# Performance work log

Hardware: AMD Instinct MI355X
Metric: run time of the kernel (lower is better)

## Reference

```python
import jax, jax.numpy as jnp
import numpy as np

P = 64        # patch size
DIM = 128     # embed dim
ROT = 64      # rotary dim (dim_head)
REC = 3       # recurrence
T = 15        # max_seq_len == conv channels
PPP = 1 * P * P  # pixels per patch


def rope_tables(H):
    # rotary-embedding-torch: inv_freq over even indices, angles repeated pairwise
    inv = 1.0 / (10000.0 ** (jnp.arange(0, ROT, 2, dtype=jnp.float32) / ROT))
    ang = jnp.arange(H, dtype=jnp.float32)[:, None] * inv[None, :]   # [H, ROT//2]
    ang = jnp.repeat(ang, 2, axis=-1)                                 # [H, ROT]
    return jnp.cos(ang), jnp.sin(ang)


def apply_rope(t, cos, sin):
    # t: [B, C, H, W]; rotate first ROT features along seq dim H
    tl = t[..., :ROT]
    x2 = tl.reshape(tl.shape[:-1] + (ROT // 2, 2))
    rot = jnp.stack([-x2[..., 1], x2[..., 0]], axis=-1).reshape(tl.shape)
    tl = tl * cos + rot * sin  # cos/sin [H, ROT] broadcast over [B, C, H, ROT]
    return jnp.concatenate([tl, t[..., ROT:]], axis=-1)


def criss_cross(x, Wq, bq, Wk, bk, Wv, bv, gamma, cos, sin, diag_mask):
    # x: [B, C, H, W] with C=T, H=n_patches, W=DIM
    q = jnp.einsum('bchw,oc->bohw', x, Wq) + bq[None, :, None, None]
    k = jnp.einsum('bchw,oc->bohw', x, Wk) + bk[None, :, None, None]
    v = jnp.einsum('bchw,oc->bohw', x, Wv) + bv[None, :, None, None]
    q = apply_rope(q, cos, sin)[:, 0]  # [B, H, W] (q/k have a single channel)
    k = apply_rope(k, cos, sin)[:, 0]
    H = x.shape[2]
    # energy_H[b,h,w,g] = q[b,h,w] * k[b,g,w]  (column attention, diag masked -inf)
    eH = jnp.einsum('bhw,bgw->bhwg', q, k) + diag_mask[None, :, None, :]
    # energy_W[b,h,w,u] = q[b,h,w] * k[b,h,u]  (row attention)
    eW = jnp.einsum('bhw,bhu->bhwu', q, k)
    att = jax.nn.softmax(jnp.concatenate([eH, eW], axis=-1), axis=-1)
    attH, attW = att[..., :H], att[..., H:]
    outH = jnp.einsum('bcgw,bhwg->bchw', v, attH)
    outW = jnp.einsum('bchu,bhwu->bchw', v, attW)
    return gamma * (outH + outW) + x


def setup_inputs() -> dict:
    key = jax.random.key(0)
    ks = jax.random.split(key, 16)
    f = lambda k, shape, s=0.05: jax.random.normal(k, shape, jnp.float32) * s
    x = jax.random.normal(ks[0], (2, T, 1, 1024, 1024), jnp.float32)
    return dict(
        x=x,
        W_emb=f(ks[1], (PPP, DIM)), b_emb=f(ks[2], (DIM,)),
        Wq=f(ks[3], (REC, 1, T)), bq=f(ks[4], (REC, 1)),
        Wk=f(ks[5], (REC, 1, T)), bk=f(ks[6], (REC, 1)),
        Wv=f(ks[7], (REC, T, T)), bv=f(ks[8], (REC, T)),
        gamma=jax.random.normal(ks[9], (REC,), jnp.float32) * 0.5,
        W_mlp=f(ks[10], (DIM, DIM)),
        W_p1=f(ks[11], (DIM, DIM)), b_p1=f(ks[12], (DIM,)),
        W_p2=f(ks[13], (DIM, PPP)), b_p2=f(ks[14], (PPP,)),
    )


def reference(x, W_emb, b_emb, Wq, bq, Wk, bk, Wv, bv, gamma, W_mlp, W_p1, b_p1, W_p2, b_p2):
    b, t, c, Hi, Wi = x.shape
    nh, nw = Hi // P, Wi // P
    Hn = nh * nw  # number of patches
    # patchify: b t c (h p1)(w p2) -> b t (h w) (c p1 p2)
    patches = x.reshape(b, t, c, nh, P, nw, P).transpose(0, 1, 3, 5, 2, 4, 6)
    patches = patches.reshape(b, t, Hn, c * P * P)
    x_e = patches @ W_emb + b_emb  # [b, t, Hn, DIM]

    cos, sin = rope_tables(Hn)
    diag_mask = jnp.where(jnp.eye(Hn, dtype=bool), -jnp.inf, 0.0).astype(jnp.float32)
    h = x_e  # interpreted as [B=b, C=t, H=Hn, W=DIM]
    for i in range(REC):
        h = criss_cross(h, Wq[i], bq[i], Wk[i], bk[i], Wv[i], bv[i], gamma[i], cos, sin, diag_mask)
    x_h = h @ W_mlp  # Linear(dim, dim, bias=False)

    def recover(z):
        p = (z @ W_p1 + b_p1) @ W_p2 + b_p2          # [b, t, Hn, PPP]
        return p.reshape(b, t, c, Hi, Wi)             # b t (d h w) -> b t d h w

    x_p = recover(x_e)
    x_h_p = recover(x_h)
    return (x_e, x_h, x_p, x_h_p)
```

## Files before the change

kernel.cpp:

```cpp
#include <hip/hip_runtime.h>
#include <math.h>

typedef __attribute__((ext_vector_type(8))) short bf16x8;
typedef __attribute__((ext_vector_type(8))) unsigned short u16x8;
typedef __attribute__((ext_vector_type(4))) unsigned short u16x4;
typedef __attribute__((ext_vector_type(4))) float f32x4;
typedef unsigned short u16;

#define XE_OFF   0
#define XH_OFF   983040
#define XP_OFF   1966080
#define XHP_OFF  33423360

#define SCR_COS   0
#define SCR_SIN   8192
#define SCR_Q     16384
#define SCR_K     81920
#define SCR_V     147456
#define SCR_HA    1130496
#define SCR_HB    2113536
#define SCR_M1    3096576
#define SCR_S1    3162112
#define SCR_AW    3227648
#define SCR_VT    4210688
#define SCR_KT    5193728
#define SCR_QT    5259264
#define SCR_OHT   5324800
#define SCR_M2    6307840
#define SCR_S2    6373376
#define SCR_PART  6438912

__device__ __forceinline__ u16 f2bf(float f) {
    unsigned u = __float_as_uint(f);
    return (u16)((u + 0x7fffu + ((u >> 16) & 1)) >> 16);
}

union U8 { u16 h[8]; bf16x8 v; u16x8 u; };

__global__ __launch_bounds__(256) void prep_k(const float* __restrict__ Wemb,
                                              const float* __restrict__ Wp1,
                                              const float* __restrict__ Wmlp,
                                              const float* __restrict__ Wp2,
                                              float* __restrict__ cosb, float* __restrict__ sinb,
                                              u16* __restrict__ Wembt, u16* __restrict__ Wp1t,
                                              u16* __restrict__ Wmlpt, u16* __restrict__ Wp2t) {
    __shared__ float tl[32][33];
    int bid = blockIdx.x, tid = threadIdx.x;
    if (bid < 32) {
        int i = bid * 256 + tid;
        int n = i >> 5, j = i & 31;
        float inv = expf(-(float)j * 0.28782313662425573f);
        float ang = (float)n * inv;
        cosb[i] = cosf(ang);
        sinb[i] = sinf(ang);
        return;
    }
    const float* in; u16* outp; int K, N, gx, gy;
    if (bid < 544)      { int i = bid - 32;  in = Wemb; outp = Wembt; K = 4096; N = 128;  gx = i & 3;   gy = i >> 2; }
    else if (bid < 560) { int i = bid - 544; in = Wp1;  outp = Wp1t;  K = 128;  N = 128;  gx = i & 3;   gy = i >> 2; }
    else if (bid < 576) { int i = bid - 560; in = Wmlp; outp = Wmlpt; K = 128;  N = 128;  gx = i & 3;   gy = i >> 2; }
    else                { int i = bid - 576; in = Wp2;  outp = Wp2t;  K = 128;  N = 4096; gx = i & 127; gy = i >> 7; }
    int n0 = gx * 32, k0 = gy * 32;
    int tx = tid & 31, ty = tid >> 5;
#pragma unroll
    for (int r = 0; r < 4; ++r)
        tl[ty + r * 8][tx] = in[(size_t)(k0 + ty + r * 8) * N + n0 + tx];
    __syncthreads();
#pragma unroll
    for (int r = 0; r < 4; ++r)
        outp[(size_t)(n0 + ty + r * 8) * K + k0 + tx] = f2bf(tl[tx][ty + r * 8]);
}

__global__ __launch_bounds__(256) void embed_mfma_k(const float* __restrict__ x,
                                                    const u16* __restrict__ Wembt,
                                                    float* __restrict__ part) {
    __shared__ char Al[64 * 128];
    __shared__ char Bl[128 * 128];
    int ck = blockIdx.x, mt = blockIdx.y;
    int m0 = mt * 64;
    int bt = m0 >> 8;
    int n0r = m0 & 255;
    const float* xb = x + (size_t)bt * 1048576;
    int tid = threadIdx.x;
    int ln = tid & 63, wv = tid >> 6;
    int wm = wv >> 1, wn = wv & 1;

    f32x4 acc[2][4];
#pragma unroll
    for (int mi = 0; mi < 2; ++mi)
#pragma unroll
        for (int ni = 0; ni < 4; ++ni) acc[mi][ni] = (f32x4){0.f, 0.f, 0.f, 0.f};

    int ar = tid & 63, aseg = tid >> 6;
    int an = n0r + ar;
    const float* arow = xb + ((size_t)(an >> 4) * 64) * 1024 + (an & 15) * 64;

    for (int bk = 0; bk < 8; ++bk) {
        int kbase = ck * 512 + bk * 64;
        __syncthreads();
        {
            const float* src = arow + (size_t)(kbase >> 6) * 1024 + aseg * 16;
            float4 f0 = ((const float4*)src)[0];
            float4 f1 = ((const float4*)src)[1];
            float4 f2 = ((const float4*)src)[2];
            float4 f3 = ((const float4*)src)[3];
            U8 u0, u1;
            u0.h[0] = f2bf(f0.x); u0.h[1] = f2bf(f0.y); u0.h[2] = f2bf(f0.z); u0.h[3] = f2bf(f0.w);
            u0.h[4] = f2bf(f1.x); u0.h[5] = f2bf(f1.y); u0.h[6] = f2bf(f1.z); u0.h[7] = f2bf(f1.w);
            u1.h[0] = f2bf(f2.x); u1.h[1] = f2bf(f2.y); u1.h[2] = f2bf(f2.z); u1.h[3] = f2bf(f2.w);
            u1.h[4] = f2bf(f3.x); u1.h[5] = f2bf(f3.y); u1.h[6] = f2bf(f3.z); u1.h[7] = f2bf(f3.w);
            int sw = (ar & 7) << 4;
            *(bf16x8*)(Al + ar * 128 + ((aseg * 32) ^ sw))      = u0.v;
            *(bf16x8*)(Al + ar * 128 + ((aseg * 32 + 16) ^ sw)) = u1.v;
        }
#pragma unroll
        for (int j = 0; j < 4; ++j) {
            int c = tid + 256 * j;
            int n = c >> 3, k0 = (c & 7) * 8;
            U8 u;
            u.u = *(const u16x8*)(Wembt + (size_t)n * 4096 + kbase + k0);
            *(bf16x8*)(Bl + n * 128 + ((k0 * 2) ^ ((n & 7) << 4))) = u.v;
        }
        __syncthreads();
#pragma unroll
        for (int ks = 0; ks < 2; ++ks) {
            int k2 = (ks * 32 + (ln >> 4) * 8) * 2;
            bf16x8 a[2], b[4];
#pragma unroll
            for (int mi = 0; mi < 2; ++mi) {
                int row = wm * 32 + mi * 16 + (ln & 15);
                a[mi] = *(const bf16x8*)(Al + row * 128 + (k2 ^ ((row & 7) << 4)));
            }
#pragma unroll
            for (int ni = 0; ni < 4; ++ni) {
                int n = wn * 64 + ni * 16 + (ln & 15);
                b[ni] = *(const bf16x8*)(Bl + n * 128 + (k2 ^ ((n & 7) << 4)));
            }
#pragma unroll
            for (int mi = 0; mi < 2; ++mi)
#pragma unroll
                for (int ni = 0; ni < 4; ++ni)
                    acc[mi][ni] = __builtin_amdgcn_mfma_f32_16x16x32_bf16(a[mi], b[ni], acc[mi][ni], 0, 0, 0);
        }
    }
    float* p = part + (size_t)ck * 983040;
#pragma unroll
    for (int mi = 0; mi < 2; ++mi)
#pragma unroll
        for (int ni = 0; ni < 4; ++ni)
#pragma unroll
            for (int r = 0; r < 4; ++r) {
                int row = m0 + wm * 32 + mi * 16 + (ln >> 4) * 4 + r;
                int col = wn * 64 + ni * 16 + (ln & 15);
                p[(size_t)row * 128 + col] = acc[mi][ni][r];
            }
}

__global__ __launch_bounds__(256) void embed_reduce_k(const float* __restrict__ part,
                                                      const float* __restrict__ bemb,
                                                      float* __restrict__ xe) {
    int i = blockIdx.x * 256 + threadIdx.x;
    const float4* p = (const float4*)part;
    float4 s = p[i];
#pragma unroll
    for (int j = 1; j < 8; ++j) {
        float4 a = p[(size_t)j * 245760 + i];
        s.x += a.x; s.y += a.y; s.z += a.z; s.w += a.w;
    }
    float4 bb = ((const float4*)bemb)[i & 31];
    s.x += bb.x; s.y += bb.y; s.z += bb.z; s.w += bb.w;
    ((float4*)xe)[i] = s;
}

template<int ABF, int OBF, int HASB>
__global__ __launch_bounds__(256) void gemm_bt_k(const void* __restrict__ Ap,
                                                 const u16* __restrict__ Bt,
                                                 const float* __restrict__ bias,
                                                 void* __restrict__ outp, int N) {
    __shared__ char Al[64 * 256];
    __shared__ char Bl[128 * 256];
    int n0 = blockIdx.x * 128, m0 = blockIdx.y * 64;
    int tid = threadIdx.x;
    int ln = tid & 63, wv = tid >> 6;
    int wm = wv >> 1, wn = wv & 1;
    {
        int row = tid >> 2, kseg = (tid & 3) * 32;
        int sw = (row & 7) << 4;
        if (ABF) {
            const u16* src = (const u16*)Ap + (size_t)(m0 + row) * 128 + kseg;
#pragma unroll
            for (int j = 0; j < 4; ++j) {
                U8 u; u.u = *(const u16x8*)(src + j * 8);
                *(bf16x8*)(Al + row * 256 + (((kseg + j * 8) * 2) ^ sw)) = u.v;
            }
        } else {
            const float* src = (const float*)Ap + (size_t)(m0 + row) * 128 + kseg;
#pragma unroll
            for (int j = 0; j < 4; ++j) {
                float4 f0 = ((const float4*)src)[2 * j];
                float4 f1 = ((const float4*)src)[2 * j + 1];
                U8 u;
                u.h[0] = f2bf(f0.x); u.h[1] = f2bf(f0.y); u.h[2] = f2bf(f0.z); u.h[3] = f2bf(f0.w);
                u.h[4] = f2bf(f1.x); u.h[5] = f2bf(f1.y); u.h[6] = f2bf(f1.z); u.h[7] = f2bf(f1.w);
                *(bf16x8*)(Al + row * 256 + (((kseg + j * 8) * 2) ^ sw)) = u.v;
            }
        }
    }
    {
        int n = tid >> 1, kseg = (tid & 1) * 64;
        int sw = (n & 7) << 4;
        const u16* src = Bt + (size_t)(n0 + n) * 128 + kseg;
#pragma unroll
        for (int j = 0; j < 8; ++j) {
            U8 u; u.u = *(const u16x8*)(src + j * 8);
            *(bf16x8*)(Bl + n * 256 + (((kseg + j * 8) * 2) ^ sw)) = u.v;
        }
    }
    __syncthreads();
    f32x4 acc[2][4];
#pragma unroll
    for (int mi = 0; mi < 2; ++mi)
#pragma unroll
        for (int ni = 0; ni < 4; ++ni) acc[mi][ni] = (f32x4){0.f, 0.f, 0.f, 0.f};
#pragma unroll
    for (int ks = 0; ks < 4; ++ks) {
        int k2 = (ks * 32 + (ln >> 4) * 8) * 2;
        bf16x8 a[2], b[4];
#pragma unroll
        for (int mi = 0; mi < 2; ++mi) {
            int row = wm * 32 + mi * 16 + (ln & 15);
            a[mi] = *(const bf16x8*)(Al + row * 256 + (k2 ^ ((row & 7) << 4)));
        }
#pragma unroll
        for (int ni = 0; ni < 4; ++ni) {
            int n = wn * 64 + ni * 16 + (ln & 15);
            b[ni] = *(const bf16x8*)(Bl + n * 256 + (k2 ^ ((n & 7) << 4)));
        }
#pragma unroll
        for (int mi = 0; mi < 2; ++mi)
#pragma unroll
            for (int ni = 0; ni < 4; ++ni)
                acc[mi][ni] = __builtin_amdgcn_mfma_f32_16x16x32_bf16(a[mi], b[ni], acc[mi][ni], 0, 0, 0);
    }
#pragma unroll
    for (int mi = 0; mi < 2; ++mi)
#pragma unroll
        for (int ni = 0; ni < 4; ++ni)
#pragma unroll
            for (int r = 0; r < 4; ++r) {
                int row = m0 + wm * 32 + mi * 16 + (ln >> 4) * 4 + r;
                int col = n0 + wn * 64 + ni * 16 + (ln & 15);
                float v = acc[mi][ni][r];
                if (HASB) v += bias[col];
                if (OBF) ((u16*)outp)[(size_t)row * N + col] = f2bf(v);
                else     ((float*)outp)[(size_t)row * N + col] = v;
            }
}

__global__ __launch_bounds__(256) void recover_k(const float* __restrict__ A,
                                                 const u16* __restrict__ Wp1t,
                                                 const float* __restrict__ bp1,
                                                 const u16* __restrict__ Wp2t,
                                                 const float* __restrict__ bp2,
                                                 float* __restrict__ outp) {
    __shared__ char Zl[64 * 256];
    __shared__ char Bl[128 * 256];
    __shared__ char Al2[64 * 256];
    int cb = blockIdx.x * 512, m0 = blockIdx.y * 64;
    int tid = threadIdx.x, ln = tid & 63, wv = tid >> 6;
    int wm = wv >> 1, wn = wv & 1;
    {
        int row = tid >> 2, kseg = (tid & 3) * 32;
        int sw = (row & 7) << 4;
        const float* src = A + (size_t)(m0 + row) * 128 + kseg;
#pragma unroll
        for (int j = 0; j < 4; ++j) {
            float4 f0 = ((const float4*)src)[2 * j];
            float4 f1 = ((const float4*)src)[2 * j + 1];
            U8 u;
            u.h[0] = f2bf(f0.x); u.h[1] = f2bf(f0.y); u.h[2] = f2bf(f0.z); u.h[3] = f2bf(f0.w);
            u.h[4] = f2bf(f1.x); u.h[5] = f2bf(f1.y); u.h[6] = f2bf(f1.z); u.h[7] = f2bf(f1.w);
            *(bf16x8*)(Al2 + row * 256 + (((kseg + j * 8) * 2) ^ sw)) = u.v;
        }
        int n = tid >> 1, ks2 = (tid & 1) * 64;
        int swb = (n & 7) << 4;
        const u16* bsrc = Wp1t + (size_t)n * 128 + ks2;
#pragma unroll
        for (int j = 0; j < 8; ++j) {
            U8 u; u.u = *(const u16x8*)(bsrc + j * 8);
            *(bf16x8*)(Bl + n * 256 + (((ks2 + j * 8) * 2) ^ swb)) = u.v;
        }
    }
    __syncthreads();
    {
        f32x4 zacc[2][4];
#pragma unroll
        for (int mi = 0; mi < 2; ++mi)
#pragma unroll
            for (int ni = 0; ni < 4; ++ni) zacc[mi][ni] = (f32x4){0.f, 0.f, 0.f, 0.f};
#pragma unroll
        for (int ks = 0; ks < 4; ++ks) {
            int k2 = (ks * 32 + (ln >> 4) * 8) * 2;
            bf16x8 a[2], b[4];
#pragma unroll
            for (int mi = 0; mi < 2; ++mi) {
                int row = wm * 32 + mi * 16 + (ln & 15);
                a[mi] = *(const bf16x8*)(Al2 + row * 256 + (k2 ^ ((row & 7) << 4)));
            }
#pragma unroll
            for (int ni = 0; ni < 4; ++ni) {
                int n = wn * 64 + ni * 16 + (ln & 15);
                b[ni] = *(const bf16x8*)(Bl + n * 256 + (k2 ^ ((n & 7) << 4)));
            }
#pragma unroll
            for (int mi = 0; mi < 2; ++mi)
#pragma unroll
                for (int ni = 0; ni < 4; ++ni)
                    zacc[mi][ni] = __builtin_amdgcn_mfma_f32_16x16x32_bf16(a[mi], b[ni], zacc[mi][ni], 0, 0, 0);
        }
#pragma unroll
        for (int ni = 0; ni < 4; ++ni) {
            int col = wn * 64 + ni * 16 + (ln & 15);
            float bb = bp1[col];
#pragma unroll
            for (int mi = 0; mi < 2; ++mi)
#pragma unroll
                for (int r = 0; r < 4; ++r) {
                    int row = wm * 32 + mi * 16 + (ln >> 4) * 4 + r;
                    *(u16*)(Zl + row * 256 + ((col * 2) ^ ((row & 7) << 4))) =
                        f2bf(zacc[mi][ni][r] + bb);
                }
        }
    }
    for (int nb = 0; nb < 4; ++nb) {
        __syncthreads();
        {
            int n = tid >> 1, ks2 = (tid & 1) * 64;
            int swb = (n & 7) << 4;
            const u16* bsrc = Wp2t + (size_t)(cb + nb * 128 + n) * 128 + ks2;
#pragma unroll
            for (int j = 0; j < 8; ++j) {
                U8 u; u.u = *(const u16x8*)(bsrc + j * 8);
                *(bf16x8*)(Bl + n * 256 + (((ks2 + j * 8) * 2) ^ swb)) = u.v;
            }
        }
        __syncthreads();
        f32x4 acc[2][4];
#pragma unroll
        for (int mi = 0; mi < 2; ++mi)
#pragma unroll
            for (int ni = 0; ni < 4; ++ni) acc[mi][ni] = (f32x4){0.f, 0.f, 0.f, 0.f};
#pragma unroll
        for (int ks = 0; ks < 4; ++ks) {
            int k2 = (ks * 32 + (ln >> 4) * 8) * 2;
            bf16x8 a[2], b[4];
#pragma unroll
            for (int mi = 0; mi < 2; ++mi) {
                int row = wm * 32 + mi * 16 + (ln & 15);
                a[mi] = *(const bf16x8*)(Zl + row * 256 + (k2 ^ ((row & 7) << 4)));
            }
#pragma unroll
            for (int ni = 0; ni < 4; ++ni) {
                int n = wn * 64 + ni * 16 + (ln & 15);
                b[ni] = *(const bf16x8*)(Bl + n * 256 + (k2 ^ ((n & 7) << 4)));
            }
#pragma unroll
            for (int mi = 0; mi < 2; ++mi)
#pragma unroll
                for (int ni = 0; ni < 4; ++ni)
                    acc[mi][ni] = __builtin_amdgcn_mfma_f32_16x16x32_bf16(a[mi], b[ni], acc[mi][ni], 0, 0, 0);
        }
#pragma unroll
        for (int ni = 0; ni < 4; ++ni) {
            int col = cb + nb * 128 + wn * 64 + ni * 16 + (ln & 15);
            float bb = bp2[col];
#pragma unroll
            for (int mi = 0; mi < 2; ++mi)
#pragma unroll
                for (int r = 0; r < 4; ++r) {
                    int row = m0 + wm * 32 + mi * 16 + (ln >> 4) * 4 + r;
                    __builtin_nontemporal_store(acc[mi][ni][r] + bb,
                                                outp + (size_t)row * 4096 + col);
                }
        }
    }
}

__global__ __launch_bounds__(128) void qkvW_k(const float* __restrict__ hin,
    const float* __restrict__ Wq, const float* __restrict__ bq,
    const float* __restrict__ Wk, const float* __restrict__ bk,
    const float* __restrict__ Wv, const float* __restrict__ bv,
    const float* __restrict__ cosb, const float* __restrict__ sinb,
    float* __restrict__ q, float* __restrict__ k, float* __restrict__ v,
    float* __restrict__ m1g, float* __restrict__ S1g, float* __restrict__ accW) {
    __shared__ char Pl[128 * 256];
    __shared__ char Vt[16 * 256];
    __shared__ float klds[128];
    __shared__ float red[2];
    __shared__ float ol[128][17];
    int b = blockIdx.x >> 8, hh = blockIdx.x & 255;
    int d = threadIdx.x;
    float hv[15];
#pragma unroll
    for (int t = 0; t < 15; ++t)
        hv[t] = hin[(((size_t)b * 15 + t) * 256 + hh) * 128 + d];
    float qp = bq[0], kp = bk[0];
#pragma unroll
    for (int t = 0; t < 15; ++t) {
        qp = fmaf(hv[t], Wq[t], qp);
        kp = fmaf(hv[t], Wk[t], kp);
    }
    float qpart = __shfl_xor(qp, 1);
    float kpart = __shfl_xor(kp, 1);
    float qo = qp, ko = kp;
    if (d < 64) {
        int j = d >> 1;
        float c = cosb[hh * 32 + j], s = sinb[hh * 32 + j];
        if (d & 1) { qo = fmaf(qp, c,  qpart * s); ko = fmaf(kp, c,  kpart * s); }
        else       { qo = fmaf(qp, c, -qpart * s); ko = fmaf(kp, c, -kpart * s); }
    }
    float vv[15];
#pragma unroll
    for (int c = 0; c < 15; ++c) {
        float a = bv[c];
#pragma unroll
        for (int t = 0; t < 15; ++t) a = fmaf(hv[t], Wv[c * 15 + t], a);
        vv[c] = a;
    }
    q[((size_t)b * 256 + hh) * 128 + d] = qo;
    k[((size_t)b * 256 + hh) * 128 + d] = ko;
#pragma unroll
    for (int c = 0; c < 15; ++c)
        v[(((size_t)b * 15 + c) * 256 + hh) * 128 + d] = vv[c];
    klds[d] = ko;
#pragma unroll
    for (int c = 0; c < 15; ++c)
        *(u16*)(Vt + ((c * 256 + d * 2) ^ ((c & 7) << 4))) = f2bf(vv[c]);
    *(u16*)(Vt + ((15 * 256 + d * 2) ^ 112)) = 0x3F80;
    float ka = fabsf(ko);
#pragma unroll
    for (int off = 32; off >= 1; off >>= 1) ka = fmaxf(ka, __shfl_xor(ka, off));
    if ((d & 63) == 0) red[d >> 6] = ka;
    __syncthreads();
    ka = fmaxf(red[0], red[1]);
    float m1 = fabsf(qo) * ka;
    m1g[((size_t)b * 256 + hh) * 128 + d] = m1;
    int swp = (d & 7) << 4;
#pragma unroll 4
    for (int u8 = 0; u8 < 128; u8 += 8) {
        f32x4 k0 = *(const f32x4*)&klds[u8];
        f32x4 k1 = *(const f32x4*)&klds[u8 + 4];
        U8 u;
        u.h[0] = f2bf(__expf(fmaf(qo, k0.x, -m1)));
        u.h[1] = f2bf(__expf(fmaf(qo, k0.y, -m1)));
        u.h[2] = f2bf(__expf(fmaf(qo, k0.z, -m1)));
        u.h[3] = f2bf(__expf(fmaf(qo, k0.w, -m1)));
        u.h[4] = f2bf(__expf(fmaf(qo, k1.x, -m1)));
        u.h[5] = f2bf(__expf(fmaf(qo, k1.y, -m1)));
        u.h[6] = f2bf(__expf(fmaf(qo, k1.z, -m1)));
        u.h[7] = f2bf(__expf(fmaf(qo, k1.w, -m1)));
        *(bf16x8*)(Pl + d * 256 + ((u8 * 2) ^ swp)) = u.v;
    }
    __syncthreads();
    int ln = d & 63, wvv = d >> 6;
    f32x4 acc[4];
#pragma unroll
    for (int mt = 0; mt < 4; ++mt) acc[mt] = (f32x4){0.f, 0.f, 0.f, 0.f};
#pragma unroll
    for (int ks = 0; ks < 4; ++ks) {
        int k2 = (ks * 32 + (ln >> 4) * 8) * 2;
        int n = ln & 15;
        bf16x8 bf = *(const bf16x8*)(Vt + n * 256 + (k2 ^ ((n & 7) << 4)));
#pragma unroll
        for (int mt = 0; mt < 4; ++mt) {
            int row = wvv * 64 + mt * 16 + (ln & 15);
            bf16x8 a = *(const bf16x8*)(Pl + row * 256 + (k2 ^ ((row & 7) << 4)));
            acc[mt] = __builtin_amdgcn_mfma_f32_16x16x32_bf16(a, bf, acc[mt], 0, 0, 0);
        }
    }
    {
        int c = ln & 15;
#pragma unroll
        for (int mt = 0; mt < 4; ++mt)
#pragma unroll
            for (int r = 0; r < 4; ++r)
                ol[wvv * 64 + mt * 16 + (ln >> 4) * 4 + r][c] = acc[mt][r];
    }
    __syncthreads();
    S1g[((size_t)b * 256 + hh) * 128 + d] = ol[d][15];
#pragma unroll
    for (int c = 0; c < 15; ++c)
        accW[(((size_t)b * 15 + c) * 256 + hh) * 128 + d] = ol[d][c];
}

__global__ __launch_bounds__(256) void trans_k(const float* __restrict__ v,
                                               const float* __restrict__ k,
                                               const float* __restrict__ q,
                                               float* __restrict__ vT,
                                               float* __restrict__ kT,
                                               float* __restrict__ qT) {
    __shared__ float tl[32][33];
    int bid = blockIdx.x, tid = threadIdx.x;
    const float* in; float* outp; int tile;
    if (bid < 960)       { int idx = bid >> 5; tile = bid & 31; in = v + (size_t)idx * 32768; outp = vT + (size_t)idx * 32768; }
    else if (bid < 1024) { int i = bid - 960;  int idx = i >> 5; tile = i & 31; in = k + (size_t)idx * 32768; outp = kT + (size_t)idx * 32768; }
    else                 { int i = bid - 1024; int idx = i >> 5; tile = i & 31; in = q + (size_t)idx * 32768; outp = qT + (size_t)idx * 32768; }
    int g0 = (tile >> 2) * 32, w0 = (tile & 3) * 32;
    int tx = tid & 31, ty = tid >> 5;
#pragma unroll
    for (int r = 0; r < 4; ++r)
        tl[ty + 8 * r][tx] = in[(size_t)(g0 + ty + 8 * r) * 128 + w0 + tx];
    __syncthreads();
#pragma unroll
    for (int r = 0; r < 4; ++r)
        outp[(size_t)(w0 + ty + 8 * r) * 256 + g0 + tx] = tl[tx][ty + 8 * r];
}

__global__ __launch_bounds__(256) void attnH_k(const float* __restrict__ qT,
    const float* __restrict__ kT, const float* __restrict__ vT,
    float* __restrict__ outHT, float* __restrict__ m2T, float* __restrict__ S2T) {
    __shared__ char Pl[256 * 128];
    __shared__ char Vl[16 * 128];
    __shared__ float klds[256];
    __shared__ float ol[256][17];
    __shared__ float kabs_s;
    int b = blockIdx.x >> 7, w = blockIdx.x & 127;
    int tid = threadIdx.x;
    if (tid < 64) {
        f32x4 kk = *(const f32x4*)(kT + ((size_t)b * 128 + w) * 256 + 4 * tid);
        *(f32x4*)&klds[4 * tid] = kk;
        float ka = fmaxf(fmaxf(fabsf(kk.x), fabsf(kk.y)), fmaxf(fabsf(kk.z), fabsf(kk.w)));
#pragma unroll
        for (int off = 32; off >= 1; off >>= 1) ka = fmaxf(ka, __shfl_xor(ka, off));
        if (tid == 0) kabs_s = ka;
    }
    float qs = qT[((size_t)b * 128 + w) * 256 + tid];
    __syncthreads();
    float m2 = fabsf(qs) * kabs_s;
    int ln = tid & 63, wv = tid >> 6;
    f32x4 acc[4];
#pragma unroll
    for (int mt = 0; mt < 4; ++mt) acc[mt] = (f32x4){0.f, 0.f, 0.f, 0.f};
    int swp = (tid & 7) << 4;
    for (int gc = 0; gc < 4; ++gc) {
        {
            int c = tid >> 4, seg = tid & 15;
            int gg = gc * 64 + seg * 4;
            u16x4 o;
            if (c < 15) {
                f32x4 vv4 = *(const f32x4*)(vT + (((size_t)b * 15 + c) * 128 + w) * 256 + gg);
                o[0] = f2bf(vv4.x); o[1] = f2bf(vv4.y); o[2] = f2bf(vv4.z); o[3] = f2bf(vv4.w);
            } else {
                o[0] = 0x3F80; o[1] = 0x3F80; o[2] = 0x3F80; o[3] = 0x3F80;
            }
            *(u16x4*)(Vl + ((c * 128 + seg * 8) ^ ((c & 7) << 4))) = o;
        }
#pragma unroll
        for (int g8 = 0; g8 < 64; g8 += 8) {
            f32x4 k0 = *(const f32x4*)&klds[gc * 64 + g8];
            f32x4 k1 = *(const f32x4*)&klds[gc * 64 + g8 + 4];
            int gbase = gc * 64 + g8;
            U8 u;
            float p0 = __expf(fmaf(qs, k0.x, -m2)); if (gbase + 0 == tid) p0 = 0.f;
            float p1 = __expf(fmaf(qs, k0.y, -m2)); if (gbase + 1 == tid) p1 = 0.f;
            float p2 = __expf(fmaf(qs, k0.z, -m2)); if (gbase + 2 == tid) p2 = 0.f;
            float p3 = __expf(fmaf(qs, k0.w, -m2)); if (gbase + 3 == tid) p3 = 0.f;
            float p4 = __expf(fmaf(qs, k1.x, -m2)); if (gbase + 4 == tid) p4 = 0.f;
            float p5 = __expf(fmaf(qs, k1.y, -m2)); if (gbase + 5 == tid) p5 = 0.f;
            float p6 = __expf(fmaf(qs, k1.z, -m2)); if (gbase + 6 == tid) p6 = 0.f;
            float p7 = __expf(fmaf(qs, k1.w, -m2)); if (gbase + 7 == tid) p7 = 0.f;
            u.h[0] = f2bf(p0); u.h[1] = f2bf(p1); u.h[2] = f2bf(p2); u.h[3] = f2bf(p3);
            u.h[4] = f2bf(p4); u.h[5] = f2bf(p5); u.h[6] = f2bf(p6); u.h[7] = f2bf(p7);
            *(bf16x8*)(Pl + tid * 128 + ((g8 * 2) ^ swp)) = u.v;
        }
        __syncthreads();
#pragma unroll
        for (int ks = 0; ks < 2; ++ks) {
            int k2 = (ks * 32 + (ln >> 4) * 8) * 2;
            int n = ln & 15;
            bf16x8 bf = *(const bf16x8*)(Vl + n * 128 + (k2 ^ ((n & 7) << 4)));
#pragma unroll
            for (int mt = 0; mt < 4; ++mt) {
                int row = wv * 64 + mt * 16 + (ln & 15);
                bf16x8 a = *(const bf16x8*)(Pl + row * 128 + (k2 ^ ((row & 7) << 4)));
                acc[mt] = __builtin_amdgcn_mfma_f32_16x16x32_bf16(a, bf, acc[mt], 0, 0, 0);
            }
        }
        __syncthreads();
    }
    {
        int c = ln & 15;
#pragma unroll
        for (int mt = 0; mt < 4; ++mt)
#pragma unroll
            for (int r = 0; r < 4; ++r)
                ol[wv * 64 + mt * 16 + (ln >> 4) * 4 + r][c] = acc[mt][r];
    }
    __syncthreads();
    size_t base = ((size_t)b * 128 + w) * 256 + tid;
    m2T[base] = m2;
    S2T[base] = ol[tid][15];
#pragma unroll
    for (int c = 0; c < 15; ++c)
        outHT[(((size_t)b * 15 + c) * 128 + w) * 256 + tid] = ol[tid][c];
}

__global__ __launch_bounds__(256) void combine_k(const float* __restrict__ hin,
    const float* __restrict__ accW, const float* __restrict__ outHT,
    const float* __restrict__ m1, const float* __restrict__ S1,
    const float* __restrict__ m2T, const float* __restrict__ S2T,
    const float* __restrict__ gptr, float* __restrict__ hout) {
    __shared__ float ot[32][33];
    __shared__ float m2l[32][33], s2l[32][33];
    int bid = blockIdx.x;
    int c = bid % 15, wt = (bid / 15) & 3, ht = (bid / 60) & 7, b = bid / 480;
    int h0 = ht * 32, w0 = wt * 32;
    int tid = threadIdx.x, tx = tid & 31, ty = tid >> 5;
#pragma unroll
    for (int r = 0; r < 4; ++r) {
        int wl = ty + 8 * r;
        size_t tb = ((size_t)b * 128 + w0 + wl) * 256 + h0 + tx;
        m2l[wl][tx] = m2T[tb];
        s2l[wl][tx] = S2T[tb];
        ot[wl][tx] = outHT[(((size_t)b * 15 + c) * 128 + w0 + wl) * 256 + h0 + tx];
    }
    __syncthreads();
    float g = gptr[0];
#pragma unroll
    for (int r = 0; r < 4; ++r) {
        int hl = ty + 8 * r;
        int h = h0 + hl, w = w0 + tx;
        size_t hw = ((size_t)b * 256 + h) * 128 + w;
        float m1v = m1[hw], S1v = S1[hw];
        float m2v = m2l[tx][hl], S2v = s2l[tx][hl];
        float mm = fmaxf(m1v, m2v);
        float e1 = __expf(m1v - mm), e2 = __expf(m2v - mm);
        float sc = g / (S1v * e1 + S2v * e2);
        size_t oi = (((size_t)b * 15 + c) * 256 + h) * 128 + w;
        hout[oi] = hin[oi] + sc * e1 * accW[oi] + sc * e2 * ot[tx][hl];
    }
}

extern "C" void kernel_launch(void* const* d_in, const int* in_sizes, int n_in,
                              void* d_out, int out_size, void* d_ws, size_t ws_size,
                              hipStream_t stream) {
    const float* x    = (const float*)d_in[0];
    const float* Wemb = (const float*)d_in[1];
    const float* bemb = (const float*)d_in[2];
    const float* Wq   = (const float*)d_in[3];
    const float* bq   = (const float*)d_in[4];
    const float* Wk   = (const float*)d_in[5];
    const float* bk   = (const float*)d_in[6];
    const float* Wv   = (const float*)d_in[7];
    const float* bv   = (const float*)d_in[8];
    const float* gam  = (const float*)d_in[9];
    const float* Wmlp = (const float*)d_in[10];
    const float* Wp1  = (const float*)d_in[11];
    const float* bp1  = (const float*)d_in[12];
    const float* Wp2  = (const float*)d_in[13];
    const float* bp2  = (const float*)d_in[14];

    float* out = (float*)d_out;
    float* xe  = out + XE_OFF;
    float* xh  = out + XH_OFF;
    float* xp  = out + XP_OFF;
    float* xhp = out + XHP_OFF;

    float* scr   = xhp;
    float* cosb  = scr + SCR_COS;
    float* sinb  = scr + SCR_SIN;
    float* qb    = scr + SCR_Q;
    float* kb    = scr + SCR_K;
    float* vb    = scr + SCR_V;
    float* ha    = scr + SCR_HA;
    float* hb    = scr + SCR_HB;
    float* m1g   = scr + SCR_M1;
    float* S1g   = scr + SCR_S1;
    float* accW  = scr + SCR_AW;
    float* vTb   = scr + SCR_VT;
    float* kTb   = scr + SCR_KT;
    float* qTb   = scr + SCR_QT;
    float* outHT = scr + SCR_OHT;
    float* m2T   = scr + SCR_M2;
    float* S2T   = scr + SCR_S2;
    float* prt   = scr + SCR_PART;
    u16* Wp2t  = (u16*)d_ws;
    u16* Wembt = (u16*)((char*)d_ws + 1048576);
    u16* Wp1t  = (u16*)((char*)d_ws + 2097152);
    u16* Wmlpt = (u16*)((char*)d_ws + 2129920);

    prep_k<<<1088, 256, 0, stream>>>(Wemb, Wp1, Wmlp, Wp2, cosb, sinb,
                                     Wembt, Wp1t, Wmlpt, Wp2t);
    embed_mfma_k<<<dim3(8, 120), 256, 0, stream>>>(x, Wembt, prt);
    embed_reduce_k<<<960, 256, 0, stream>>>(prt, bemb, xe);

    const float* hin = xe;
    float* houts[3] = {ha, hb, ha};
    for (int i = 0; i < 3; ++i) {
        qkvW_k<<<512, 128, 0, stream>>>(hin, Wq + i * 15, bq + i, Wk + i * 15, bk + i,
                                        Wv + i * 225, bv + i * 15, cosb, sinb,
                                        qb, kb, vb, m1g, S1g, accW);
        trans_k<<<1088, 256, 0, stream>>>(vb, kb, qb, vTb, kTb, qTb);
        attnH_k<<<256, 256, 0, stream>>>(qTb, kTb, vTb, outHT, m2T, S2T);
        combine_k<<<1536, 256, 0, stream>>>(hin, accW, outHT, m1g, S1g, m2T, S2T,
                                            gam + i, houts[i]);
        hin = houts[i];
    }

    gemm_bt_k<0, 0, 0><<<dim3(1, 120), 256, 0, stream>>>(hin, Wmlpt, nullptr, xh, 128);
    recover_k<<<dim3(8, 120), 256, 0, stream>>>(xe, Wp1t, bp1, Wp2t, bp2, xp);
    recover_k<<<dim3(8, 120), 256, 0, stream>>>(xh, Wp1t, bp1, Wp2t, bp2, xhp);
}
```

Before: 232.3 us.

## Split attention kernels across more threads and blocks for occupancy

qkvW_k now runs 256 threads per block: one half computes q/k with RoPE while the other computes v, and the exp/MFMA work is split between the halves. attnH_k splits the key dimension into two halves across twice as many blocks. Each half writes its own partial output and sum buffers, and combine_k adds them. This raises parallelism on a GPU that is underfilled with only 256–512 blocks, at the cost of extra scratch traffic and an additional read in combine.

```diff
diff --git a/kernel.cpp b/kernel.cpp
--- a/kernel.cpp
+++ b/kernel.cpp
@@ -28,7 +28,9 @@
 #define SCR_OHT   5324800
 #define SCR_M2    6307840
 #define SCR_S2    6373376
-#define SCR_PART  6438912
+#define SCR_OHT1  6438912
+#define SCR_S21   7421952
+#define SCR_PART  7487488
 
 __device__ __forceinline__ u16 f2bf(float f) {
     unsigned u = __float_as_uint(f);
@@ -386,7 +388,7 @@
     }
 }
 
-__global__ __launch_bounds__(128) void qkvW_k(const float* __restrict__ hin,
+__global__ __launch_bounds__(256) void qkvW_k(const float* __restrict__ hin,
     const float* __restrict__ Wq, const float* __restrict__ bq,
     const float* __restrict__ Wk, const float* __restrict__ bk,
     const float* __restrict__ Wv, const float* __restrict__ bv,
@@ -396,60 +398,73 @@
     __shared__ char Pl[128 * 256];
     __shared__ char Vt[16 * 256];
     __shared__ float klds[128];
+    __shared__ float qlds[128];
     __shared__ float red[2];
     __shared__ float ol[128][17];
     int b = blockIdx.x >> 8, hh = blockIdx.x & 255;
-    int d = threadIdx.x;
-    float hv[15];
-#pragma unroll
-    for (int t = 0; t < 15; ++t)
-        hv[t] = hin[(((size_t)b * 15 + t) * 256 + hh) * 128 + d];
-    float qp = bq[0], kp = bk[0];
-#pragma unroll
-    for (int t = 0; t < 15; ++t) {
-        qp = fmaf(hv[t], Wq[t], qp);
-        kp = fmaf(hv[t], Wk[t], kp);
-    }
-    float qpart = __shfl_xor(qp, 1);
-    float kpart = __shfl_xor(kp, 1);
-    float qo = qp, ko = kp;
-    if (d < 64) {
-        int j = d >> 1;
-        float c = cosb[hh * 32 + j], s = sinb[hh * 32 + j];
-        if (d & 1) { qo = fmaf(qp, c,  qpart * s); ko = fmaf(kp, c,  kpart * s); }
-        else       { qo = fmaf(qp, c, -qpart * s); ko = fmaf(kp, c, -kpart * s); }
-    }
-    float vv[15];
-#pragma unroll
-    for (int c = 0; c < 15; ++c) {
-        float a = bv[c];
-#pragma unroll
-        for (int t = 0; t < 15; ++t) a = fmaf(hv[t], Wv[c * 15 + t], a);
-        vv[c] = a;
-    }
-    q[((size_t)b * 256 + hh) * 128 + d] = qo;
-    k[((size_t)b * 256 + hh) * 128 + d] = ko;
-#pragma unroll
-    for (int c = 0; c < 15; ++c)
-        v[(((size_t)b * 15 + c) * 256 + hh) * 128 + d] = vv[c];
-    klds[d] = ko;
-#pragma unroll
-    for (int c = 0; c < 15; ++c)
-        *(u16*)(Vt + ((c * 256 + d * 2) ^ ((c & 7) << 4))) = f2bf(vv[c]);
-    *(u16*)(Vt + ((15 * 256 + d * 2) ^ 112)) = 0x3F80;
-    float ka = fabsf(ko);
-#pragma unroll
-    for (int off = 32; off >= 1; off >>= 1) ka = fmaxf(ka, __shfl_xor(ka, off));
-    if ((d & 63) == 0) red[d >> 6] = ka;
-    __syncthreads();
-    ka = fmaxf(red[0], red[1]);
+    int tid = threadIdx.x;
+    int d = tid & 127, half = tid >> 7;
+
+    if (half == 0) {
+        float hv[15];
+#pragma unroll
+        for (int t = 0; t < 15; ++t)
+            hv[t] = hin[(((size_t)b * 15 + t) * 256 + hh) * 128 + d];
+        float qp = bq[0], kp = bk[0];
+#pragma unroll
+        for (int t = 0; t < 15; ++t) {
+            qp = fmaf(hv[t], Wq[t], qp);
+            kp = fmaf(hv[t], Wk[t], kp);
+        }
+        float qpart = __shfl_xor(qp, 1);
+        float kpart = __shfl_xor(kp, 1);
+        float qo = qp, ko = kp;
+        if (d < 64) {
+            int j = d >> 1;
+            float c = cosb[hh * 32 + j], s = sinb[hh * 32 + j];
+            if (d & 1) { qo = fmaf(qp, c,  qpart * s); ko = fmaf(kp, c,  kpart * s); }
+            else       { qo = fmaf(qp, c, -qpart * s); ko = fmaf(kp, c, -kpart * s); }
+        }
+        q[((size_t)b * 256 + hh) * 128 + d] = qo;
+        k[((size_t)b * 256 + hh) * 128 + d] = ko;
+        klds[d] = ko;
+        qlds[d] = qo;
+        float ka = fabsf(ko);
+#pragma unroll
+        for (int off = 32; off >= 1; off >>= 1) ka = fmaxf(ka, __shfl_xor(ka, off));
+        if ((tid & 63) == 0) red[tid >> 6] = ka;
+    } else {
+        float hv[15];
+#pragma unroll
+        for (int t = 0; t < 15; ++t)
+            hv[t] = hin[(((size_t)b * 15 + t) * 256 + hh) * 128 + d];
+        float vv[15];
+#pragma unroll
+        for (int c = 0; c < 15; ++c) {
+            float a = bv[c];
+#pragma unroll
+            for (int t = 0; t < 15; ++t) a = fmaf(hv[t], Wv[c * 15 + t], a);
+            vv[c] = a;
+        }
+#pragma unroll
+        for (int c = 0; c < 15; ++c)
+            v[(((size_t)b * 15 + c) * 256 + hh) * 128 + d] = vv[c];
+#pragma unroll
+        for (int c = 0; c < 15; ++c)
+            *(u16*)(Vt + ((c * 256 + d * 2) ^ ((c & 7) << 4))) = f2bf(vv[c]);
+        *(u16*)(Vt + ((15 * 256 + d * 2) ^ 112)) = 0x3F80;
+    }
+    __syncthreads();
+    float ka = fmaxf(red[0], red[1]);
+    float qo = qlds[d];
     float m1 = fabsf(qo) * ka;
-    m1g[((size_t)b * 256 + hh) * 128 + d] = m1;
+    if (half == 0) m1g[((size_t)b * 256 + hh) * 128 + d] = m1;
     int swp = (d & 7) << 4;
+    int u0 = half * 64;
 #pragma unroll 4
-    for (int u8 = 0; u8 < 128; u8 += 8) {
-        f32x4 k0 = *(const f32x4*)&klds[u8];
-        f32x4 k1 = *(const f32x4*)&klds[u8 + 4];
+    for (int u8 = 0; u8 < 64; u8 += 8) {
+        f32x4 k0 = *(const f32x4*)&klds[u0 + u8];
+        f32x4 k1 = *(const f32x4*)&klds[u0 + u8 + 4];
         U8 u;
         u.h[0] = f2bf(__expf(fmaf(qo, k0.x, -m1)));
         u.h[1] = f2bf(__expf(fmaf(qo, k0.y, -m1)));
@@ -459,21 +474,21 @@
         u.h[5] = f2bf(__expf(fmaf(qo, k1.y, -m1)));
         u.h[6] = f2bf(__expf(fmaf(qo, k1.z, -m1)));
         u.h[7] = f2bf(__expf(fmaf(qo, k1.w, -m1)));
-        *(bf16x8*)(Pl + d * 256 + ((u8 * 2) ^ swp)) = u.v;
-    }
-    __syncthreads();
-    int ln = d & 63, wvv = d >> 6;
-    f32x4 acc[4];
-#pragma unroll
-    for (int mt = 0; mt < 4; ++mt) acc[mt] = (f32x4){0.f, 0.f, 0.f, 0.f};
+        *(bf16x8*)(Pl + d * 256 + (((u0 + u8) * 2) ^ swp)) = u.v;
+    }
+    __syncthreads();
+    int ln = tid & 63, wvv = tid >> 6;
+    f32x4 acc[2];
+    acc[0] = (f32x4){0.f, 0.f, 0.f, 0.f};
+    acc[1] = (f32x4){0.f, 0.f, 0.f, 0.f};
 #pragma unroll
     for (int ks = 0; ks < 4; ++ks) {
         int k2 = (ks * 32 + (ln >> 4) * 8) * 2;
         int n = ln & 15;
         bf16x8 bf = *(const bf16x8*)(Vt + n * 256 + (k2 ^ ((n & 7) << 4)));
 #pragma unroll
-        for (int mt = 0; mt < 4; ++mt) {
-            int row = wvv * 64 + mt * 16 + (ln & 15);
+        for (int mt = 0; mt < 2; ++mt) {
+            int row = wvv * 32 + mt * 16 + (ln & 15);
             bf16x8 a = *(const bf16x8*)(Pl + row * 256 + (k2 ^ ((row & 7) << 4)));
             acc[mt] = __builtin_amdgcn_mfma_f32_16x16x32_bf16(a, bf, acc[mt], 0, 0, 0);
         }
@@ -481,16 +496,17 @@
     {
         int c = ln & 15;
 #pragma unroll
-        for (int mt = 0; mt < 4; ++mt)
+        for (int mt = 0; mt < 2; ++mt)
 #pragma unroll
             for (int r = 0; r < 4; ++r)
-                ol[wvv * 64 + mt * 16 + (ln >> 4) * 4 + r][c] = acc[mt][r];
-    }
-    __syncthreads();
-    S1g[((size_t)b * 256 + hh) * 128 + d] = ol[d][15];
-#pragma unroll
-    for (int c = 0; c < 15; ++c)
-        accW[(((size_t)b * 15 + c) * 256 + hh) * 128 + d] = ol[d][c];
+                ol[wvv * 32 + mt * 16 + (ln >> 4) * 4 + r][c] = acc[mt][r];
+    }
+    __syncthreads();
+    if (half == 0) S1g[((size_t)b * 256 + hh) * 128 + d] = ol[d][15];
+    for (int e = tid; e < 1920; e += 256) {
+        int c = e >> 7, w = e & 127;
+        accW[(((size_t)b * 15 + c) * 256 + hh) * 128 + w] = ol[w][c];
+    }
 }
 
 __global__ __launch_bounds__(256) void trans_k(const float* __restrict__ v,
@@ -518,13 +534,16 @@
 
 __global__ __launch_bounds__(256) void attnH_k(const float* __restrict__ qT,
     const float* __restrict__ kT, const float* __restrict__ vT,
-    float* __restrict__ outHT, float* __restrict__ m2T, float* __restrict__ S2T) {
+    float* __restrict__ outHT0, float* __restrict__ outHT1,
+    float* __restrict__ m2T, float* __restrict__ S2T0, float* __restrict__ S2T1) {
     __shared__ char Pl[256 * 128];
     __shared__ char Vl[16 * 128];
     __shared__ float klds[256];
     __shared__ float ol[256][17];
     __shared__ float kabs_s;
-    int b = blockIdx.x >> 7, w = blockIdx.x & 127;
+    int bid = blockIdx.x;
+    int b = bid >> 8, rem = bid & 255;
+    int w = rem >> 1, gh = rem & 1;
     int tid = threadIdx.x;
     if (tid < 64) {
         f32x4 kk = *(const f32x4*)(kT + ((size_t)b * 128 + w) * 256 + 4 * tid);
@@ -542,10 +561,11 @@
 #pragma unroll
     for (int mt = 0; mt < 4; ++mt) acc[mt] = (f32x4){0.f, 0.f, 0.f, 0.f};
     int swp = (tid & 7) << 4;
-    for (int gc = 0; gc < 4; ++gc) {
+    for (int gc = 0; gc < 2; ++gc) {
+        int gbase0 = gh * 128 + gc * 64;
         {
             int c = tid >> 4, seg = tid & 15;
-            int gg = gc * 64 + seg * 4;
+            int gg = gbase0 + seg * 4;
             u16x4 o;
             if (c < 15) {
                 f32x4 vv4 = *(const f32x4*)(vT + (((size_t)b * 15 + c) * 128 + w) * 256 + gg);
@@ -557,9 +577,9 @@
         }
 #pragma unroll
         for (int g8 = 0; g8 < 64; g8 += 8) {
-            f32x4 k0 = *(const f32x4*)&klds[gc * 64 + g8];
-            f32x4 k1 = *(const f32x4*)&klds[gc * 64 + g8 + 4];
-            int gbase = gc * 64 + g8;
+            f32x4 k0 = *(const f32x4*)&klds[gbase0 + g8];
+            f32x4 k1 = *(const f32x4*)&klds[gbase0 + g8 + 4];
+            int gbase = gbase0 + g8;
             U8 u;
             float p0 = __expf(fmaf(qs, k0.x, -m2)); if (gbase + 0 == tid) p0 = 0.f;
             float p1 = __expf(fmaf(qs, k0.y, -m2)); if (gbase + 1 == tid) p1 = 0.f;
@@ -598,17 +618,21 @@
     }
     __syncthreads();
     size_t base = ((size_t)b * 128 + w) * 256 + tid;
-    m2T[base] = m2;
-    S2T[base] = ol[tid][15];
+    if (gh == 0) m2T[base] = m2;
+    float* s2 = gh ? S2T1 : S2T0;
+    float* oht = gh ? outHT1 : outHT0;
+    s2[base] = ol[tid][15];
 #pragma unroll
     for (int c = 0; c < 15; ++c)
-        outHT[(((size_t)b * 15 + c) * 128 + w) * 256 + tid] = ol[tid][c];
+        oht[(((size_t)b * 15 + c) * 128 + w) * 256 + tid] = ol[tid][c];
 }
 
 __global__ __launch_bounds__(256) void combine_k(const float* __restrict__ hin,
-    const float* __restrict__ accW, const float* __restrict__ outHT,
+    const float* __restrict__ accW,
+    const float* __restrict__ outHT0, const float* __restrict__ outHT1,
     const float* __restrict__ m1, const float* __restrict__ S1,
-    const float* __restrict__ m2T, const float* __restrict__ S2T,
+    const float* __restrict__ m2T,
+    const float* __restrict__ S2T0, const float* __restrict__ S2T1,
     const float* __restrict__ gptr, float* __restrict__ hout) {
     __shared__ float ot[32][33];
     __shared__ float m2l[32][33], s2l[32][33];
@@ -620,9 +644,10 @@
     for (int r = 0; r < 4; ++r) {
         int wl = ty + 8 * r;
         size_t tb = ((size_t)b * 128 + w0 + wl) * 256 + h0 + tx;
+        size_t ob = (((size_t)b * 15 + c) * 128 + w0 + wl) * 256 + h0 + tx;
         m2l[wl][tx] = m2T[tb];
-        s2l[wl][tx] = S2T[tb];
-        ot[wl][tx] = outHT[(((size_t)b * 15 + c) * 128 + w0 + wl) * 256 + h0 + tx];
+        s2l[wl][tx] = S2T0[tb] + S2T1[tb];
+        ot[wl][tx] = outHT0[ob] + outHT1[ob];
     }
     __syncthreads();
     float g = gptr[0];
@@ -666,24 +691,26 @@
     float* xp  = out + XP_OFF;
     float* xhp = out + XHP_OFF;
 
-    float* scr   = xhp;
-    float* cosb  = scr + SCR_COS;
-    float* sinb  = scr + SCR_SIN;
-    float* qb    = scr + SCR_Q;
-    float* kb    = scr + SCR_K;
-    float* vb    = scr + SCR_V;
-    float* ha    = scr + SCR_HA;
-    float* hb    = scr + SCR_HB;
-    float* m1g   = scr + SCR_M1;
-    float* S1g   = scr + SCR_S1;
-    float* accW  = scr + SCR_AW;
-    float* vTb   = scr + SCR_VT;
-    float* kTb   = scr + SCR_KT;
-    float* qTb   = scr + SCR_QT;
-    float* outHT = scr + SCR_OHT;
-    float* m2T   = scr + SCR_M2;
-    float* S2T   = scr + SCR_S2;
-    float* prt   = scr + SCR_PART;
+    float* scr    = xhp;
+    float* cosb   = scr + SCR_COS;
+    float* sinb   = scr + SCR_SIN;
+    float* qb     = scr + SCR_Q;
+    float* kb     = scr + SCR_K;
+    float* vb     = scr + SCR_V;
+    float* ha     = scr + SCR_HA;
+    float* hb     = scr + SCR_HB;
+    float* m1g    = scr + SCR_M1;
+    float* S1g    = scr + SCR_S1;
+    float* accW   = scr + SCR_AW;
+    float* vTb    = scr + SCR_VT;
+    float* kTb    = scr + SCR_KT;
+    float* qTb    = scr + SCR_QT;
+    float* outHT0 = scr + SCR_OHT;
+    float* m2T    = scr + SCR_M2;
+    float* S2T0   = scr + SCR_S2;
+    float* outHT1 = scr + SCR_OHT1;
+    float* S2T1   = scr + SCR_S21;
+    float* prt    = scr + SCR_PART;
     u16* Wp2t  = (u16*)d_ws;
     u16* Wembt = (u16*)((char*)d_ws + 1048576);
     u16* Wp1t  = (u16*)((char*)d_ws + 2097152);
@@ -697,13 +724,13 @@
     const float* hin = xe;
     float* houts[3] = {ha, hb, ha};
     for (int i = 0; i < 3; ++i) {
-        qkvW_k<<<512, 128, 0, stream>>>(hin, Wq + i * 15, bq + i, Wk + i * 15, bk + i,
+        qkvW_k<<<512, 256, 0, stream>>>(hin, Wq + i * 15, bq + i, Wk + i * 15, bk + i,
                                         Wv + i * 225, bv + i * 15, cosb, sinb,
                                         qb, kb, vb, m1g, S1g, accW);
         trans_k<<<1088, 256, 0, stream>>>(vb, kb, qb, vTb, kTb, qTb);
-        attnH_k<<<256, 256, 0, stream>>>(qTb, kTb, vTb, outHT, m2T, S2T);
-        combine_k<<<1536, 256, 0, stream>>>(hin, accW, outHT, m1g, S1g, m2T, S2T,
-                                            gam + i, houts[i]);
+        attnH_k<<<512, 256, 0, stream>>>(qTb, kTb, vTb, outHT0, outHT1, m2T, S2T0, S2T1);
+        combine_k<<<1536, 256, 0, stream>>>(hin, accW, outHT0, outHT1, m1g, S1g,
+                                            m2T, S2T0, S2T1, gam + i, houts[i]);
         hin = houts[i];
     }
 
```

Result: faster. 222.8 us (-4.1%).
